# Kernel optimization log

Measured on AMD Instinct MI355X. Metric: run time of the kernel, lower is better.

The kernel has to match this reference:

```python
import jax, jax.numpy as jnp
import numpy as np

B, S, D, H = 4, 2048, 1024, 16
HD = D // H
DFF = 4 * D
EPS = 1e-5


def gelu_tanh(x):
    c = jnp.sqrt(jnp.asarray(2.0 / jnp.pi, x.dtype))
    return 0.5 * x * (1.0 + jnp.tanh(c * (x + 0.044715 * x ** 3)))


def layernorm(x, scale, shift):
    mean = jnp.mean(x, axis=-1, keepdims=True)
    var = jnp.var(x, axis=-1, keepdims=True)  # unbiased=False
    return scale * (x - mean) * jax.lax.rsqrt(var + EPS) + shift


def setup_inputs() -> dict:
    key = jax.random.key(0)
    ks = jax.random.split(key, 12)
    s_in = 1.0 / np.sqrt(D)
    s_ff = 1.0 / np.sqrt(DFF)
    return {
        "x": jax.random.normal(ks[0], (B, S, D), jnp.float32),
        "Wq": jax.random.uniform(ks[1], (D, D), jnp.float32, -s_in, s_in),
        "Wk": jax.random.uniform(ks[2], (D, D), jnp.float32, -s_in, s_in),
        "Wv": jax.random.uniform(ks[3], (D, D), jnp.float32, -s_in, s_in),
        "Wo": jax.random.uniform(ks[4], (D, D), jnp.float32, -s_in, s_in),
        "bo": jax.random.uniform(ks[5], (D,), jnp.float32, -s_in, s_in),
        "W1": jax.random.uniform(ks[6], (D, DFF), jnp.float32, -s_in, s_in),
        "b1": jax.random.uniform(ks[7], (DFF,), jnp.float32, -s_in, s_in),
        "W2": jax.random.uniform(ks[8], (DFF, D), jnp.float32, -s_ff, s_ff),
        "b2": jax.random.uniform(ks[9], (D,), jnp.float32, -s_ff, s_ff),
        "ln1_scale": jnp.ones((D,), jnp.float32),
        "ln1_shift": jnp.zeros((D,), jnp.float32),
        "ln2_scale": jnp.ones((D,), jnp.float32),
        "ln2_shift": jnp.zeros((D,), jnp.float32),
    }


def reference(x, Wq, Wk, Wv, Wo, bo, W1, b1, W2, b2,
              ln1_scale, ln1_shift, ln2_scale, ln2_shift):
    # --- pre-LN causal MHA ---
    h = layernorm(x, ln1_scale, ln1_shift)
    q = (h @ Wq).reshape(B, S, H, HD).transpose(0, 2, 1, 3)  # [B,H,S,hd]
    k = (h @ Wk).reshape(B, S, H, HD).transpose(0, 2, 1, 3)
    v = (h @ Wv).reshape(B, S, H, HD).transpose(0, 2, 1, 3)
    scores = jnp.einsum('bhqd,bhkd->bhqk', q, k)
    causal = jnp.tril(jnp.ones((S, S), bool))  # mask strict upper triangle
    scores = jnp.where(causal, scores, -jnp.inf)
    attn = jax.nn.softmax(scores / np.sqrt(HD), axis=-1)
    ctx = jnp.einsum('bhqk,bhkd->bhqd', attn, v)
    ctx = ctx.transpose(0, 2, 1, 3).reshape(B, S, D)
    x = x + (ctx @ Wo + bo)
    # --- FFN ---
    h = layernorm(x, ln2_scale, ln2_shift)
    h = gelu_tanh(h @ W1 + b1) @ W2 + b2
    return x + h
```

## Files before the change

### kernel.cpp

```cpp
#include <hip/hip_runtime.h>
#include <math.h>

#define S_LEN  2048
#define DMODEL 1024
#define NHEAD  16
#define BATCH  4
#define NROWS  (BATCH*S_LEN)
#define DFF    4096
#define QKV_LD 3072

typedef __attribute__((ext_vector_type(4))) unsigned short us4;
typedef __attribute__((ext_vector_type(8))) unsigned short us8;
typedef __attribute__((ext_vector_type(8))) __bf16 bf16x8;
typedef __attribute__((ext_vector_type(4))) float f32x4;

#if __has_builtin(__builtin_amdgcn_exp2f)
#define EXP2(x) __builtin_amdgcn_exp2f(x)
#else
#define EXP2(x) exp2f(x)
#endif
#if __has_builtin(__builtin_amdgcn_rcpf)
#define RCP(x) __builtin_amdgcn_rcpf(x)
#else
#define RCP(x) (1.0f/(x))
#endif

static __device__ __forceinline__ unsigned short f2bf(float f) {
  __bf16 b = (__bf16)f;
  return __builtin_bit_cast(unsigned short, b);
}
#define GLD16(gp, lp) __builtin_amdgcn_global_load_lds( \
    (const __attribute__((address_space(1))) unsigned int*)(gp), \
    (__attribute__((address_space(3))) unsigned int*)(lp), 16, 0, 0)

__global__ __launch_bounds__(256) void ln_kernel(
    const float* __restrict__ x, const float* __restrict__ scale,
    const float* __restrict__ shift, unsigned short* __restrict__ out)
{
  const int row = blockIdx.x, tid = threadIdx.x;
  const int lane = tid & 63, wave = tid >> 6;
  const float* xr = x + (size_t)row * DMODEL;
  f32x4 v = *(const f32x4*)&xr[tid * 4];
  float s  = v[0]+v[1]+v[2]+v[3];
  float s2 = v[0]*v[0]+v[1]*v[1]+v[2]*v[2]+v[3]*v[3];
  #pragma unroll
  for (int m = 1; m < 64; m <<= 1) { s += __shfl_xor(s, m); s2 += __shfl_xor(s2, m); }
  __shared__ float red[8];
  if (lane == 0) { red[wave] = s; red[4 + wave] = s2; }
  __syncthreads();
  s  = red[0]+red[1]+red[2]+red[3];
  s2 = red[4]+red[5]+red[6]+red[7];
  float mean = s * (1.0f/DMODEL);
  float var  = s2 * (1.0f/DMODEL) - mean*mean;
  float rstd = rsqrtf(var + 1e-5f);
  us4 o;
  #pragma unroll
  for (int j = 0; j < 4; j++) {
    float val = (v[j]-mean)*rstd*scale[tid*4+j] + shift[tid*4+j];
    o[j] = f2bf(val);
  }
  *(us4*)&out[(size_t)row*DMODEL + tid*4] = o;
}

__global__ __launch_bounds__(256) void wtrans_all(
    const float* __restrict__ Wq, const float* __restrict__ Wk,
    const float* __restrict__ Wv, const float* __restrict__ Wo,
    const float* __restrict__ W1, const float* __restrict__ W2,
    unsigned short* __restrict__ wqkvt, unsigned short* __restrict__ wot,
    unsigned short* __restrict__ w1t, unsigned short* __restrict__ w2t,
    float sclq)
{
  __shared__ unsigned short tile[64][72];
  const int bid = blockIdx.x, tid = threadIdx.x;
  const float* W; unsigned short* Wt; int K, N, sub; float scl = 1.0f;
  if (bid < 1024) {
    int wsel = bid >> 8; sub = bid & 255; K = 1024; N = 1024;
    W  = (wsel == 0) ? Wq : (wsel == 1) ? Wk : (wsel == 2) ? Wv : Wo;
    Wt = (wsel == 0) ? wqkvt : (wsel == 1) ? wqkvt + 1024*1024
       : (wsel == 2) ? wqkvt + 2048*1024 : wot;
    if (wsel == 0) scl = sclq;
  } else if (bid < 2048) { sub = bid - 1024; K = 1024; N = 4096; W = W1; Wt = w1t; }
  else                   { sub = bid - 2048; K = 4096; N = 1024; W = W2; Wt = w2t; }
  const int nbn = N >> 6;
  const int kt = sub / nbn, nt = sub % nbn;
  int r = tid >> 2, c0 = (tid & 3) << 4;
  const float* src = W + (size_t)(kt*64 + r)*N + nt*64 + c0;
  #pragma unroll
  for (int j = 0; j < 16; j += 4) {
    f32x4 f = *(const f32x4*)&src[j];
    tile[r][c0+j+0] = f2bf(f[0]*scl); tile[r][c0+j+1] = f2bf(f[1]*scl);
    tile[r][c0+j+2] = f2bf(f[2]*scl); tile[r][c0+j+3] = f2bf(f[3]*scl);
  }
  __syncthreads();
  int n = tid >> 2, k0 = (tid & 3) << 4;
  us8 o0, o1;
  #pragma unroll
  for (int j = 0; j < 8; j++) { o0[j] = tile[k0+j][n]; o1[j] = tile[k0+8+j][n]; }
  unsigned short* dst = Wt + (size_t)(nt*64 + n)*K + kt*64 + k0;
  *(us8*)&dst[0] = o0;
  *(us8*)&dst[8] = o1;
}

__global__ __launch_bounds__(256) void vtrans(
    const unsigned short* __restrict__ v, unsigned short* __restrict__ vt)
{
  __shared__ unsigned short tile[64][72];
  const int tid = threadIdx.x;
  const int bh = blockIdx.x >> 5, st = blockIdx.x & 31;
  const int b = bh >> 4, h = bh & 15;
  int r = tid >> 2, c0 = (tid & 3) << 4;
  const unsigned short* src = v + (size_t)(b*S_LEN + st*64 + r)*QKV_LD + h*64 + c0;
  *(us8*)&tile[r][c0]   = *(const us8*)&src[0];
  *(us8*)&tile[r][c0+8] = *(const us8*)&src[8];
  __syncthreads();
  int d = tid >> 2, s0 = (tid & 3) << 4;
  us8 o0, o1;
  #pragma unroll
  for (int j = 0; j < 8; j++) { o0[j] = tile[s0+j][d]; o1[j] = tile[s0+8+j][d]; }
  unsigned short* dst = vt + (size_t)(bh*64 + d)*S_LEN + st*64 + s0;
  *(us8*)&dst[0] = o0;
  *(us8*)&dst[8] = o1;
}

template<int BN, bool BIAS, bool GELU_, bool RESID, bool OUTF32>
__global__ __launch_bounds__(512, 2) void gemm256(
    const unsigned short* __restrict__ A, const unsigned short* __restrict__ Bt,
    void* Cout, const float* __restrict__ bias, const float* resid,
    int M, int N, int K)
{
  constexpr int WN = BN / 4;
  constexpr int NF = WN / 16;
  __shared__ unsigned short sA[2][256*64];
  __shared__ unsigned short sB[2][BN*64];
  const int tid = threadIdx.x;
  const int wave = tid >> 6, lane = tid & 63;
  const int wm = wave >> 2, wn = wave & 3;
  const int l15 = lane & 15, g = lane >> 4, x7 = lane & 7, r8 = lane >> 3;
  const int srcc = (x7 ^ r8) << 3;
  const int nbn = N / BN;
  const int bm = blockIdx.x / nbn, bn = blockIdx.x % nbn;
  const unsigned short* gA = A  + (size_t)(bm*256)*K;
  const unsigned short* gB = Bt + (size_t)(bn*BN)*K;
  const int NT = K >> 6;

  f32x4 acc[8][NF] = {};

#define STAGEA(buf, h, kb) do { \
    _Pragma("unroll") \
    for (int j_ = 0; j_ < 2; j_++) \
      GLD16(gA + (size_t)((h)*128 + j_*64 + wave*8 + r8)*K + (kb) + srcc, \
            &sA[buf][((h)*128 + j_*64 + wave*8)*64]); \
  } while (0)
#define STAGEB(buf, h, kb) do { \
    if (BN == 256) { \
      _Pragma("unroll") \
      for (int j_ = 0; j_ < 2; j_++) \
        GLD16(gB + (size_t)((h)*128 + j_*64 + wave*8 + r8)*K + (kb) + srcc, \
              &sB[buf][((h)*128 + j_*64 + wave*8)*64]); \
    } else { \
      GLD16(gB + (size_t)((h)*64 + wave*8 + r8)*K + (kb) + srcc, \
            &sB[buf][((h)*64 + wave*8)*64]); \
    } \
  } while (0)
#define RDA_(m, kk) (*(const bf16x8*)&cA[(wm*128 + (m)*16 + l15)*64 + ((((kk)*4+g)^x7)<<3)])
#define RDB_(n, kk) (*(const bf16x8*)&cB[(wn*WN + (n)*16 + l15)*64 + ((((kk)*4+g)^x7)<<3)])
#define PH(p) do { \
    __builtin_amdgcn_s_setprio(1); \
    _Pragma("unroll") for (int mm_ = 0; mm_ < 2; mm_++) \
    _Pragma("unroll") for (int n_ = 0; n_ < NF; n_++) \
    _Pragma("unroll") for (int kk_ = 0; kk_ < 2; kk_++) \
      acc[(p)*2+mm_][n_] = __builtin_amdgcn_mfma_f32_16x16x32_bf16( \
          af[mm_][kk_], bfr[n_][kk_], acc[(p)*2+mm_][n_], 0, 0, 0); \
    __builtin_amdgcn_s_setprio(0); \
  } while (0)

  STAGEB(0, 0, 0); STAGEB(0, 1, 0);
  STAGEA(0, 0, 0); STAGEA(0, 1, 0);
  STAGEB(1, 0, 64); STAGEB(1, 1, 64);

  for (int t = 0; t < NT; ++t) {
    const int c = t & 1;
    const unsigned short* cA = sA[c];
    const unsigned short* cB = sB[c];
    const int kb1 = (t + 1) * 64, kb2 = (t + 2) * 64;
    bf16x8 af[2][2], bfr[NF][2];

    if (t < NT - 1) {
      if constexpr (BN == 256) asm volatile("s_waitcnt vmcnt(4)" ::: "memory");
      else                     asm volatile("s_waitcnt vmcnt(2)" ::: "memory");
    } else {
      asm volatile("s_waitcnt vmcnt(0)" ::: "memory");
    }
    __builtin_amdgcn_s_barrier();
    __builtin_amdgcn_sched_barrier(0);

    #pragma unroll
    for (int n = 0; n < NF; n++) { bfr[n][0] = RDB_(n, 0); bfr[n][1] = RDB_(n, 1); }
    af[0][0] = RDA_(0, 0); af[0][1] = RDA_(0, 1);
    af[1][0] = RDA_(1, 0); af[1][1] = RDA_(1, 1);
    if (t + 1 < NT) STAGEA(c ^ 1, 0, kb1);
    PH(0);
    af[0][0] = RDA_(2, 0); af[0][1] = RDA_(2, 1);
    af[1][0] = RDA_(3, 0); af[1][1] = RDA_(3, 1);
    if (t + 1 < NT) STAGEA(c ^ 1, 1, kb1);
    PH(1);
    __builtin_amdgcn_s_barrier();
    af[0][0] = RDA_(4, 0); af[0][1] = RDA_(4, 1);
    af[1][0] = RDA_(5, 0); af[1][1] = RDA_(5, 1);
    if (t + 2 < NT) STAGEB(c, 0, kb2);
    PH(2);
    af[0][0] = RDA_(6, 0); af[0][1] = RDA_(6, 1);
    af[1][0] = RDA_(7, 0); af[1][1] = RDA_(7, 1);
    if (t + 2 < NT) STAGEB(c, 1, kb2);
    PH(3);
  }

  #pragma unroll
  for (int m = 0; m < 8; m++) {
    #pragma unroll
    for (int r = 0; r < 4; r++) {
      int grow = bm*256 + wm*128 + m*16 + g*4 + r;
      #pragma unroll
      for (int n = 0; n < NF; n++) {
        int gcol = bn*BN + wn*WN + n*16 + l15;
        float v = acc[m][n][r];
        if (BIAS) v += bias[gcol];
        if (GELU_) {
          float xx = v;
          float u = 0.7978845608f*(xx + 0.044715f*xx*xx*xx);
          float e = EXP2(u * 2.88539008f);
          float th = 1.0f - 2.0f*RCP(e + 1.0f);
          v = 0.5f*xx*(1.0f + th);
        }
        if (RESID) v += resid[(size_t)grow*N + gcol];
        if (OUTF32) ((float*)Cout)[(size_t)grow*N + gcol] = v;
        else ((unsigned short*)Cout)[(size_t)grow*N + gcol] = f2bf(v);
      }
    }
  }
#undef STAGEA
#undef STAGEB
#undef RDA_
#undef RDB_
#undef PH
}

__global__ __launch_bounds__(512) void attn_kernel(
    const unsigned short* __restrict__ qb, const unsigned short* __restrict__ kb,
    const unsigned short* __restrict__ vt, unsigned short* __restrict__ ctx)
{
  __shared__ unsigned short sK[2][64*64];
  __shared__ unsigned short sV[2][64*64];
  __shared__ unsigned short sP[8][16*64];
  const int tid = threadIdx.x, wave = tid >> 6, lane = tid & 63;
  const int l15 = lane & 15, g = lane >> 4, x7 = lane & 7;
  const int qt = 15 - (blockIdx.x >> 6);
  const int bh = blockIdx.x & 63;
  const int b = bh >> 4, h = bh & 15;
  const int qrow = qt*128 + wave*16;
  const int NTI = 2*qt + 2;

  bf16x8 qf[2];
  {
    const unsigned short* qr = qb + (size_t)(b*S_LEN + qrow + l15) * QKV_LD + h*64;
    qf[0] = *(const bf16x8*)&qr[g*8];
    qf[1] = *(const bf16x8*)&qr[32 + g*8];
  }

  f32x4 oacc[4] = {};
  float mrow[4], lrow[4];
  #pragma unroll
  for (int r = 0; r < 4; r++) { mrow[r] = -INFINITY; lrow[r] = 0.0f; }

  const int rrow = lane >> 3;
  const int srcc = (x7 ^ rrow) << 3;
  const unsigned short* kbase = kb + (size_t)(b*S_LEN)*QKV_LD + h*64 + srcc;
  const unsigned short* vbase = vt + (size_t)(bh*64)*S_LEN + srcc;

#define ASTAGE(buf, t) do { \
    const int kv0_ = (t)*64; \
    GLD16(kbase + (size_t)(kv0_ + wave*8 + rrow)*QKV_LD, &sK[buf][wave*8*64]); \
    GLD16(vbase + (size_t)(wave*8 + rrow)*S_LEN + kv0_,  &sV[buf][wave*8*64]); \
  } while(0)

  ASTAGE(0, 0);

  for (int t = 0; t < NTI; ++t) {
    __syncthreads();
    const int cur = t & 1;
    if (t < NTI - 1) ASTAGE(cur ^ 1, t + 1);

    const int kv0 = t*64;
    if (kv0 > qrow + 15) continue;

    f32x4 sacc[4] = {};
    __builtin_amdgcn_s_setprio(1);
    #pragma unroll
    for (int kk = 0; kk < 2; kk++) {
      const int csw = ((kk*4 + g) ^ x7) << 3;
      #pragma unroll
      for (int n = 0; n < 4; n++) {
        bf16x8 kf = *(const bf16x8*)&sK[cur][(n*16 + l15)*64 + csw];
        sacc[n] = __builtin_amdgcn_mfma_f32_16x16x32_bf16(qf[kk], kf, sacc[n], 0, 0, 0);
      }
    }
    __builtin_amdgcn_s_setprio(0);

    float p[4][4], gm[4];
    const bool masked = (kv0 + 63 > qrow);
    #pragma unroll
    for (int r = 0; r < 4; r++) {
      float rm = -INFINITY;
      #pragma unroll
      for (int n = 0; n < 4; n++) {
        float sc = sacc[n][r];
        if (masked && (kv0 + n*16 + l15) > (qrow + g*4 + r)) sc = -INFINITY;
        p[n][r] = sc;
        rm = fmaxf(rm, sc);
      }
      rm = fmaxf(rm, __shfl_xor(rm, 1));
      rm = fmaxf(rm, __shfl_xor(rm, 2));
      rm = fmaxf(rm, __shfl_xor(rm, 4));
      rm = fmaxf(rm, __shfl_xor(rm, 8));
      gm[r] = rm;
    }
    bool need = (gm[0] > mrow[0] + 8.0f) | (gm[1] > mrow[1] + 8.0f) |
                (gm[2] > mrow[2] + 8.0f) | (gm[3] > mrow[3] + 8.0f);
    if (__any(need)) {
      #pragma unroll
      for (int r = 0; r < 4; r++) {
        float mn = fmaxf(mrow[r], gm[r]);
        float alpha = EXP2(mrow[r] - mn);
        mrow[r] = mn;
        lrow[r] *= alpha;
        #pragma unroll
        for (int nd = 0; nd < 4; nd++) oacc[nd][r] *= alpha;
      }
    }
    #pragma unroll
    for (int r = 0; r < 4; r++) {
      float sum = 0.0f;
      #pragma unroll
      for (int n = 0; n < 4; n++) {
        float e = EXP2(p[n][r] - mrow[r]);
        p[n][r] = e;
        sum += e;
      }
      sum += __shfl_xor(sum, 1);
      sum += __shfl_xor(sum, 2);
      sum += __shfl_xor(sum, 4);
      sum += __shfl_xor(sum, 8);
      lrow[r] += sum;
    }

    #pragma unroll
    for (int n = 0; n < 4; n++) {
      const int chunk = n*2 + (l15 >> 3);
      #pragma unroll
      for (int r = 0; r < 4; r++) {
        const int prow = g*4 + r;
        sP[wave][prow*64 + ((chunk ^ (prow & 7)) << 3) + x7] = f2bf(p[n][r]);
      }
    }
    asm volatile("s_waitcnt lgkmcnt(0)" ::: "memory");
    __builtin_amdgcn_sched_barrier(0);

    __builtin_amdgcn_s_setprio(1);
    #pragma unroll
    for (int kk = 0; kk < 2; kk++) {
      const int csw = ((kk*4 + g) ^ x7) << 3;
      bf16x8 pa = *(const bf16x8*)&sP[wave][l15*64 + csw];
      #pragma unroll
      for (int nd = 0; nd < 4; nd++) {
        bf16x8 vf = *(const bf16x8*)&sV[cur][(nd*16 + l15)*64 + csw];
        oacc[nd] = __builtin_amdgcn_mfma_f32_16x16x32_bf16(pa, vf, oacc[nd], 0, 0, 0);
      }
    }
    __builtin_amdgcn_s_setprio(0);
  }

  #pragma unroll
  for (int r = 0; r < 4; r++) {
    float inv = 1.0f / lrow[r];
    size_t row = (size_t)(b*S_LEN + qrow + g*4 + r);
    #pragma unroll
    for (int nd = 0; nd < 4; nd++)
      ctx[row*DMODEL + h*64 + nd*16 + l15] = f2bf(oacc[nd][r] * inv);
  }
}

extern "C" void kernel_launch(void* const* d_in, const int* in_sizes, int n_in,
                              void* d_out, int out_size, void* d_ws, size_t ws_size,
                              hipStream_t stream)
{
  const float* x    = (const float*)d_in[0];
  const float* Wq   = (const float*)d_in[1];
  const float* Wk   = (const float*)d_in[2];
  const float* Wv   = (const float*)d_in[3];
  const float* Wo   = (const float*)d_in[4];
  const float* bo   = (const float*)d_in[5];
  const float* W1   = (const float*)d_in[6];
  const float* b1   = (const float*)d_in[7];
  const float* W2   = (const float*)d_in[8];
  const float* b2   = (const float*)d_in[9];
  const float* ln1s = (const float*)d_in[10];
  const float* ln1b = (const float*)d_in[11];
  const float* ln2s = (const float*)d_in[12];
  const float* ln2b = (const float*)d_in[13];
  float* out = (float*)d_out;
  (void)in_sizes; (void)n_in; (void)out_size; (void)ws_size;

  char* ws = (char*)d_ws;
  size_t off = 0;
  auto alloc = [&](size_t n) { char* p = ws + off; off += (n + 255) & ~(size_t)255; return p; };
  unsigned short* hbuf  = (unsigned short*)alloc((size_t)NROWS*DMODEL*2);
  unsigned short* qkv   = (unsigned short*)alloc((size_t)NROWS*QKV_LD*2);
  unsigned short* vtb   = (unsigned short*)alloc((size_t)NROWS*DMODEL*2);
  unsigned short* ctx   = (unsigned short*)alloc((size_t)NROWS*DMODEL*2);
  unsigned short* ffn1  = (unsigned short*)alloc((size_t)NROWS*DFF*2);
  unsigned short* wqkvt = (unsigned short*)alloc((size_t)QKV_LD*DMODEL*2);
  unsigned short* wot   = (unsigned short*)alloc((size_t)DMODEL*DMODEL*2);
  unsigned short* w1t   = (unsigned short*)alloc((size_t)DFF*DMODEL*2);
  unsigned short* w2t   = (unsigned short*)alloc((size_t)DMODEL*DFF*2);

  const float SCLQ = 0.18033688011f;

  wtrans_all<<<dim3(3072), dim3(256), 0, stream>>>(
      Wq, Wk, Wv, Wo, W1, W2, wqkvt, wot, w1t, w2t, SCLQ);

  ln_kernel<<<dim3(NROWS), dim3(256), 0, stream>>>(x, ln1s, ln1b, hbuf);
  gemm256<256,false,false,false,false><<<dim3(32*12), dim3(512), 0, stream>>>(
      hbuf, wqkvt, (void*)qkv, nullptr, nullptr, NROWS, QKV_LD, DMODEL);
  vtrans<<<dim3(2048), dim3(256), 0, stream>>>(qkv + 2048, vtb);
  attn_kernel<<<dim3(1024), dim3(512), 0, stream>>>(qkv, qkv + 1024, vtb, ctx);
  gemm256<128,true,false,true,true><<<dim3(32*8), dim3(512), 0, stream>>>(
      ctx, wot, (void*)out, bo, x, NROWS, DMODEL, DMODEL);
  ln_kernel<<<dim3(NROWS), dim3(256), 0, stream>>>(out, ln2s, ln2b, hbuf);
  gemm256<256,true,true,false,false><<<dim3(32*16), dim3(512), 0, stream>>>(
      hbuf, w1t, (void*)ffn1, b1, nullptr, NROWS, DFF, DMODEL);
  gemm256<128,true,false,true,true><<<dim3(32*8), dim3(512), 0, stream>>>(
      ffn1, w2t, (void*)out, b2, out, NROWS, DMODEL, DFF);
}
```

Baseline: 432.7 us.

## Add 128x128 GEMM for N=1024 outputs, XCD swizzle, MFMA row-sum in attention

Adds a simpler 128x128-tile GEMM with 256 threads and 3 blocks per CU, used for the Wo and W2 projections, which gives 512 blocks instead of 256. Remaps block IDs across the 8 XCDs so neighbouring tiles share L2. In attention, the softmax row sum is now computed by an extra MFMA against a ones vector, and the row-max shuffle reduction runs only when a rescale is needed. The new GEMM is single-buffered with no prefetch, so global-load latency may be exposed.

```diff
diff --git a/kernel.cpp b/kernel.cpp
--- a/kernel.cpp
+++ b/kernel.cpp
@@ -32,6 +32,11 @@
 #define GLD16(gp, lp) __builtin_amdgcn_global_load_lds( \
     (const __attribute__((address_space(1))) unsigned int*)(gp), \
     (__attribute__((address_space(3))) unsigned int*)(lp), 16, 0, 0)
+
+static __device__ __forceinline__ int xcd_swz(int bid, int nwg) {
+  int q = nwg >> 3;
+  return (bid & 7) * q + (bid >> 3);
+}
 
 __global__ __launch_bounds__(256) void ln_kernel(
     const float* __restrict__ x, const float* __restrict__ scale,
@@ -122,14 +127,88 @@
   *(us8*)&dst[8] = o1;
 }
 
-template<int BN, bool BIAS, bool GELU_, bool RESID, bool OUTF32>
-__global__ __launch_bounds__(512, 2) void gemm256(
+template<bool BIAS, bool RESID, bool GELU_, bool OUTF32>
+__global__ __launch_bounds__(256, 3) void gemm_bt(
     const unsigned short* __restrict__ A, const unsigned short* __restrict__ Bt,
     void* Cout, const float* __restrict__ bias, const float* resid,
     int M, int N, int K)
 {
-  constexpr int WN = BN / 4;
-  constexpr int NF = WN / 16;
+  __shared__ unsigned short sA[128*64];
+  __shared__ unsigned short sB[128*64];
+  const int tid = threadIdx.x;
+  const int wave = tid >> 6, lane = tid & 63;
+  const int l15 = lane & 15, g = lane >> 4, x7 = lane & 7;
+  const int nbn = N >> 7;
+  const int bid = xcd_swz(blockIdx.x, gridDim.x);
+  const int bm = bid / nbn, bn = bid % nbn;
+  const int wr = (wave >> 1) << 6, wc = (wave & 1) << 6;
+
+  f32x4 acc[4][4] = {};
+
+  const int rrow = lane >> 3;
+  const int srcc = (x7 ^ rrow) << 3;
+  const unsigned short* ga0 = A  + (size_t)(bm*128 + rrow)*K + srcc;
+  const unsigned short* gb0 = Bt + (size_t)(bn*128 + rrow)*K + srcc;
+
+  for (int kb = 0; kb < K; kb += 64) {
+    #pragma unroll
+    for (int i = 0; i < 4; i++) {
+      int rr = (wave*4 + i) * 8;
+      GLD16(ga0 + (size_t)rr*K + kb, &sA[rr*64]);
+      GLD16(gb0 + (size_t)rr*K + kb, &sB[rr*64]);
+    }
+    __syncthreads();
+    #pragma unroll
+    for (int kk = 0; kk < 2; kk++) {
+      const int csw = ((kk*4 + g) ^ x7) << 3;
+      bf16x8 af[4], bfr[4];
+      #pragma unroll
+      for (int m = 0; m < 4; m++)
+        af[m] = *(const bf16x8*)&sA[(wr + m*16 + l15)*64 + csw];
+      #pragma unroll
+      for (int n = 0; n < 4; n++)
+        bfr[n] = *(const bf16x8*)&sB[(wc + n*16 + l15)*64 + csw];
+      #pragma unroll
+      for (int m = 0; m < 4; m++)
+        #pragma unroll
+        for (int n = 0; n < 4; n++)
+          acc[m][n] = __builtin_amdgcn_mfma_f32_16x16x32_bf16(af[m], bfr[n], acc[m][n], 0, 0, 0);
+    }
+    __syncthreads();
+  }
+
+  #pragma unroll
+  for (int m = 0; m < 4; m++) {
+    #pragma unroll
+    for (int r = 0; r < 4; r++) {
+      int grow = bm*128 + wr + m*16 + g*4 + r;
+      #pragma unroll
+      for (int n = 0; n < 4; n++) {
+        int gcol = bn*128 + wc + n*16 + l15;
+        float v = acc[m][n][r];
+        if (BIAS) v += bias[gcol];
+        if (GELU_) {
+          float xx = v;
+          float u = 0.7978845608f*(xx + 0.044715f*xx*xx*xx);
+          float e = EXP2(u * 2.88539008f);
+          float th = 1.0f - 2.0f*RCP(e + 1.0f);
+          v = 0.5f*xx*(1.0f + th);
+        }
+        if (RESID) v += resid[(size_t)grow*N + gcol];
+        if (OUTF32) ((float*)Cout)[(size_t)grow*N + gcol] = v;
+        else ((unsigned short*)Cout)[(size_t)grow*N + gcol] = f2bf(v);
+      }
+    }
+  }
+}
+
+template<bool BIAS, bool GELU_>
+__global__ __launch_bounds__(512, 2) void gemm256(
+    const unsigned short* __restrict__ A, const unsigned short* __restrict__ Bt,
+    unsigned short* __restrict__ Cout, const float* __restrict__ bias,
+    int M, int N, int K)
+{
+  constexpr int BN = 256, WN = 64, NF = 4;
   __shared__ unsigned short sA[2][256*64];
   __shared__ unsigned short sB[2][BN*64];
   const int tid = threadIdx.x;
@@ -138,7 +217,8 @@
   const int l15 = lane & 15, g = lane >> 4, x7 = lane & 7, r8 = lane >> 3;
   const int srcc = (x7 ^ r8) << 3;
   const int nbn = N / BN;
-  const int bm = blockIdx.x / nbn, bn = blockIdx.x % nbn;
+  const int bid = xcd_swz(blockIdx.x, gridDim.x);
+  const int bm = bid / nbn, bn = bid % nbn;
   const unsigned short* gA = A  + (size_t)(bm*256)*K;
   const unsigned short* gB = Bt + (size_t)(bn*BN)*K;
   const int NT = K >> 6;
@@ -152,15 +232,10 @@
             &sA[buf][((h)*128 + j_*64 + wave*8)*64]); \
   } while (0)
 #define STAGEB(buf, h, kb) do { \
-    if (BN == 256) { \
-      _Pragma("unroll") \
-      for (int j_ = 0; j_ < 2; j_++) \
-        GLD16(gB + (size_t)((h)*128 + j_*64 + wave*8 + r8)*K + (kb) + srcc, \
-              &sB[buf][((h)*128 + j_*64 + wave*8)*64]); \
-    } else { \
-      GLD16(gB + (size_t)((h)*64 + wave*8 + r8)*K + (kb) + srcc, \
-            &sB[buf][((h)*64 + wave*8)*64]); \
-    } \
+    _Pragma("unroll") \
+    for (int j_ = 0; j_ < 2; j_++) \
+      GLD16(gB + (size_t)((h)*128 + j_*64 + wave*8 + r8)*K + (kb) + srcc, \
+            &sB[buf][((h)*128 + j_*64 + wave*8)*64]); \
   } while (0)
 #define RDA_(m, kk) (*(const bf16x8*)&cA[(wm*128 + (m)*16 + l15)*64 + ((((kk)*4+g)^x7)<<3)])
 #define RDB_(n, kk) (*(const bf16x8*)&cB[(wn*WN + (n)*16 + l15)*64 + ((((kk)*4+g)^x7)<<3)])
@@ -185,12 +260,8 @@
     const int kb1 = (t + 1) * 64, kb2 = (t + 2) * 64;
     bf16x8 af[2][2], bfr[NF][2];
 
-    if (t < NT - 1) {
-      if constexpr (BN == 256) asm volatile("s_waitcnt vmcnt(4)" ::: "memory");
-      else                     asm volatile("s_waitcnt vmcnt(2)" ::: "memory");
-    } else {
-      asm volatile("s_waitcnt vmcnt(0)" ::: "memory");
-    }
+    if (t < NT - 1) asm volatile("s_waitcnt vmcnt(4)" ::: "memory");
+    else            asm volatile("s_waitcnt vmcnt(0)" ::: "memory");
     __builtin_amdgcn_s_barrier();
     __builtin_amdgcn_sched_barrier(0);
 
@@ -232,9 +303,7 @@
           float th = 1.0f - 2.0f*RCP(e + 1.0f);
           v = 0.5f*xx*(1.0f + th);
         }
-        if (RESID) v += resid[(size_t)grow*N + gcol];
-        if (OUTF32) ((float*)Cout)[(size_t)grow*N + gcol] = v;
-        else ((unsigned short*)Cout)[(size_t)grow*N + gcol] = f2bf(v);
+        Cout[(size_t)grow*N + gcol] = f2bf(v);
       }
     }
   }
@@ -267,10 +336,16 @@
     qf[1] = *(const bf16x8*)&qr[32 + g*8];
   }
 
+  us8 ones_u;
+  #pragma unroll
+  for (int j = 0; j < 8; j++) ones_u[j] = 0x3F80;
+  const bf16x8 ones8 = __builtin_bit_cast(bf16x8, ones_u);
+
   f32x4 oacc[4] = {};
-  float mrow[4], lrow[4];
-  #pragma unroll
-  for (int r = 0; r < 4; r++) { mrow[r] = -INFINITY; lrow[r] = 0.0f; }
+  f32x4 lacc = {};
+  float mrow[4];
+  #pragma unroll
+  for (int r = 0; r < 4; r++) mrow[r] = -INFINITY;
 
   const int rrow = lane >> 3;
   const int srcc = (x7 ^ rrow) << 3;
@@ -306,52 +381,43 @@
     }
     __builtin_amdgcn_s_setprio(0);
 
-    float p[4][4], gm[4];
+    float p[4][4], rm[4];
     const bool masked = (kv0 + 63 > qrow);
     #pragma unroll
     for (int r = 0; r < 4; r++) {
-      float rm = -INFINITY;
+      float m_ = -INFINITY;
       #pragma unroll
       for (int n = 0; n < 4; n++) {
         float sc = sacc[n][r];
         if (masked && (kv0 + n*16 + l15) > (qrow + g*4 + r)) sc = -INFINITY;
         p[n][r] = sc;
-        rm = fmaxf(rm, sc);
-      }
-      rm = fmaxf(rm, __shfl_xor(rm, 1));
-      rm = fmaxf(rm, __shfl_xor(rm, 2));
-      rm = fmaxf(rm, __shfl_xor(rm, 4));
-      rm = fmaxf(rm, __shfl_xor(rm, 8));
-      gm[r] = rm;
-    }
-    bool need = (gm[0] > mrow[0] + 8.0f) | (gm[1] > mrow[1] + 8.0f) |
-                (gm[2] > mrow[2] + 8.0f) | (gm[3] > mrow[3] + 8.0f);
+        m_ = fmaxf(m_, sc);
+      }
+      rm[r] = m_;
+    }
+    bool need = (rm[0] > mrow[0] + 8.0f) | (rm[1] > mrow[1] + 8.0f) |
+                (rm[2] > mrow[2] + 8.0f) | (rm[3] > mrow[3] + 8.0f);
     if (__any(need)) {
       #pragma unroll
       for (int r = 0; r < 4; r++) {
-        float mn = fmaxf(mrow[r], gm[r]);
+        float vv = rm[r];
+        vv = fmaxf(vv, __shfl_xor(vv, 1));
+        vv = fmaxf(vv, __shfl_xor(vv, 2));
+        vv = fmaxf(vv, __shfl_xor(vv, 4));
+        vv = fmaxf(vv, __shfl_xor(vv, 8));
+        float mn = fmaxf(mrow[r], vv);
         float alpha = EXP2(mrow[r] - mn);
         mrow[r] = mn;
-        lrow[r] *= alpha;
+        lacc[r] *= alpha;
         #pragma unroll
         for (int nd = 0; nd < 4; nd++) oacc[nd][r] *= alpha;
       }
     }
     #pragma unroll
-    for (int r = 0; r < 4; r++) {
-      float sum = 0.0f;
-      #pragma unroll
-      for (int n = 0; n < 4; n++) {
-        float e = EXP2(p[n][r] - mrow[r]);
-        p[n][r] = e;
-        sum += e;
-      }
-      sum += __shfl_xor(sum, 1);
-      sum += __shfl_xor(sum, 2);
-      sum += __shfl_xor(sum, 4);
-      sum += __shfl_xor(sum, 8);
-      lrow[r] += sum;
-    }
+    for (int n = 0; n < 4; n++)
+      #pragma unroll
+      for (int r = 0; r < 4; r++)
+        p[n][r] = EXP2(p[n][r] - mrow[r]);
 
     #pragma unroll
     for (int n = 0; n < 4; n++) {
@@ -375,13 +441,14 @@
         bf16x8 vf = *(const bf16x8*)&sV[cur][(nd*16 + l15)*64 + csw];
         oacc[nd] = __builtin_amdgcn_mfma_f32_16x16x32_bf16(pa, vf, oacc[nd], 0, 0, 0);
       }
+      lacc = __builtin_amdgcn_mfma_f32_16x16x32_bf16(pa, ones8, lacc, 0, 0, 0);
     }
     __builtin_amdgcn_s_setprio(0);
   }
 
   #pragma unroll
   for (int r = 0; r < 4; r++) {
-    float inv = 1.0f / lrow[r];
+    float inv = RCP(lacc[r]);
     size_t row = (size_t)(b*S_LEN + qrow + g*4 + r);
     #pragma unroll
     for (int nd = 0; nd < 4; nd++)
@@ -429,15 +496,15 @@
       Wq, Wk, Wv, Wo, W1, W2, wqkvt, wot, w1t, w2t, SCLQ);
 
   ln_kernel<<<dim3(NROWS), dim3(256), 0, stream>>>(x, ln1s, ln1b, hbuf);
-  gemm256<256,false,false,false,false><<<dim3(32*12), dim3(512), 0, stream>>>(
-      hbuf, wqkvt, (void*)qkv, nullptr, nullptr, NROWS, QKV_LD, DMODEL);
+  gemm256<false,false><<<dim3(32*12), dim3(512), 0, stream>>>(
+      hbuf, wqkvt, qkv, nullptr, NROWS, QKV_LD, DMODEL);
   vtrans<<<dim3(2048), dim3(256), 0, stream>>>(qkv + 2048, vtb);
   attn_kernel<<<dim3(1024), dim3(512), 0, stream>>>(qkv, qkv + 1024, vtb, ctx);
-  gemm256<128,true,false,true,true><<<dim3(32*8), dim3(512), 0, stream>>>(
+  gemm_bt<true,true,false,true><<<dim3(64*8), dim3(256), 0, stream>>>(
       ctx, wot, (void*)out, bo, x, NROWS, DMODEL, DMODEL);
   ln_kernel<<<dim3(NROWS), dim3(256), 0, stream>>>(out, ln2s, ln2b, hbuf);
-  gemm256<256,true,true,false,false><<<dim3(32*16), dim3(512), 0, stream>>>(
-      hbuf, w1t, (void*)ffn1, b1, nullptr, NROWS, DFF, DMODEL);
-  gemm256<128,true,false,true,true><<<dim3(32*8), dim3(512), 0, stream>>>(
+  gemm256<true,true><<<dim3(32*16), dim3(512), 0, stream>>>(
+      hbuf, w1t, ffn1, b1, NROWS, DFF, DMODEL);
+  gemm_bt<true,true,false,true><<<dim3(64*8), dim3(256), 0, stream>>>(
       ffn1, w2t, (void*)out, b2, out, NROWS, DMODEL, DFF);
 }
```

Result: faster. 371.0 us (-14.3%).
